# Kernel tuning notes

Hardware: AMD Instinct MI355X
Metric: run time of the kernel (lower is better)

## Reference

```python
import jax, jax.numpy as jnp
import numpy as np
from math import exp

WINDOW_SIZE = 11
SIGMA = 1.5
L_VAL = 1.0


def _make_window(window_size=WINDOW_SIZE, sigma=SIGMA):
    g = np.array([exp(-(x - window_size // 2) ** 2 / float(2 * sigma ** 2))
                  for x in range(window_size)], dtype=np.float32)
    g = g / g.sum()
    w2d = np.outer(g, g).astype(np.float32)  # [K,K]
    return jnp.asarray(w2d)


def _depthwise_gauss(x, w2d):
    # x: [B,C,H,W]; w2d: [K,K]. Depthwise (grouped) conv, SAME padding.
    C = x.shape[1]
    K = w2d.shape[0]
    kern = jnp.broadcast_to(w2d[None, None], (C, 1, K, K))  # OIHW, groups=C
    pad = K // 2
    return jax.lax.conv_general_dilated(
        x, kern,
        window_strides=(1, 1),
        padding=[(pad, pad), (pad, pad)],
        dimension_numbers=('NCHW', 'OIHW', 'NCHW'),
        feature_group_count=C)


def setup_inputs() -> dict:
    key = jax.random.key(0)
    k1, k2 = jax.random.split(key)
    shape = (16, 3, 512, 512)
    img1 = jax.random.uniform(k1, shape, dtype=jnp.float32)
    img2 = jax.random.uniform(k2, shape, dtype=jnp.float32)
    return {"img1": img1, "img2": img2}


def reference(img1, img2):
    w2d = _make_window().astype(img1.dtype)
    mu1 = _depthwise_gauss(img1, w2d)
    mu2 = _depthwise_gauss(img2, w2d)
    mu1_sq = mu1 * mu1
    mu2_sq = mu2 * mu2
    mu1_mu2 = mu1 * mu2
    sigma1_sq = _depthwise_gauss(img1 * img1, w2d) - mu1_sq
    sigma2_sq = _depthwise_gauss(img2 * img2, w2d) - mu2_sq
    sigma12 = _depthwise_gauss(img1 * img2, w2d) - mu1_mu2
    C1 = (0.01 * L_VAL) ** 2
    C2 = (0.03 * L_VAL) ** 2
    ssim_map = ((2 * mu1_mu2 + C1) * (2 * sigma12 + C2)) / \
               ((mu1_sq + mu2_sq + C1) * (sigma1_sq + sigma2_sq + C2))
    return 1.0 - jnp.mean(ssim_map)  # asloss=True, reduction='mean'
```

## Files before the change

### kernel.cpp

```cpp
#include <hip/hip_runtime.h>
#include <math.h>


#define KW 11
#define RAD 5
#define TILE_W 64
#define TILE_H 32
#define IN_W (TILE_W + 2 * RAD)
#define IN_H (TILE_H + 2 * RAD)
#define S_STRIDE 76
#define H_STRIDE 65
#define IMG_H 512
#define IMG_W 512
#define NPLANES 48
#define TILES_X (IMG_W / TILE_W)
#define TILES_Y (IMG_H / TILE_H)
#define NBLOCKS (TILES_X * TILES_Y * NPLANES)
#define NPIX (16.0f * 3.0f * 512.0f * 512.0f)

struct GaussW { float g[KW]; };

__global__ __launch_bounds__(256, 2) void ssim_tile(
    const float* __restrict__ img1, const float* __restrict__ img2,
    float* __restrict__ partial, GaussW W)
{
    __shared__ float s1[IN_H][S_STRIDE];
    __shared__ float s2[IN_H][S_STRIDE];
    __shared__ float h[5][IN_H][H_STRIDE];
    __shared__ float red[4];

    const int tid = threadIdx.x;
    const int plane = blockIdx.y;
    const int tile = blockIdx.x;
    const int tx = tile & (TILES_X - 1);
    const int ty = tile >> 3;
    const int c0 = tx * TILE_W;
    const int r0 = ty * TILE_H;
    const float* __restrict__ p1 = img1 + (size_t)plane * IMG_H * IMG_W;
    const float* __restrict__ p2 = img2 + (size_t)plane * IMG_H * IMG_W;

    for (int idx = tid; idx < IN_H * IN_W; idx += 256) {
        int row = idx / IN_W;
        int col = idx - row * IN_W;
        int gr = r0 - RAD + row;
        int gc = c0 - RAD + col;
        float v1 = 0.f, v2 = 0.f;
        if ((unsigned)gr < (unsigned)IMG_H && (unsigned)gc < (unsigned)IMG_W) {
            v1 = p1[gr * IMG_W + gc];
            v2 = p2[gr * IMG_W + gc];
        }
        s1[row][col] = v1;
        s2[row][col] = v2;
    }
    __syncthreads();

    {
        const int cg = (tid & 7) * 8;
        const int row0 = tid >> 3;
        for (int rr = 0; rr < 2; ++rr) {
            const int row = row0 + rr * 32;
            if (row < IN_H) {
                float ax[8]  = {0,0,0,0,0,0,0,0};
                float ay[8]  = {0,0,0,0,0,0,0,0};
                float axx[8] = {0,0,0,0,0,0,0,0};
                float ayy[8] = {0,0,0,0,0,0,0,0};
                float axy[8] = {0,0,0,0,0,0,0,0};
                #pragma unroll
                for (int j = 0; j < 18; ++j) {
                    float x = s1[row][cg + j];
                    float y = s2[row][cg + j];
                    float xx = x * x, yy = y * y, xy = x * y;
                    #pragma unroll
                    for (int o = 0; o < 8; ++o) {
                        const int t = j - o;
                        if (t >= 0 && t < KW) {
                            const float w = W.g[t];
                            ax[o]  += w * x;
                            ay[o]  += w * y;
                            axx[o] += w * xx;
                            ayy[o] += w * yy;
                            axy[o] += w * xy;
                        }
                    }
                }
                #pragma unroll
                for (int o = 0; o < 8; ++o) {
                    const int col = cg + o;
                    h[0][row][col] = ax[o];
                    h[1][row][col] = ay[o];
                    h[2][row][col] = axx[o];
                    h[3][row][col] = ayy[o];
                    h[4][row][col] = axy[o];
                }
            }
        }
    }
    __syncthreads();

    const int col = tid & 63;
    const int rbase = (tid >> 6) * 8;
    float ox[8]  = {0,0,0,0,0,0,0,0};
    float oy[8]  = {0,0,0,0,0,0,0,0};
    float oxx[8] = {0,0,0,0,0,0,0,0};
    float oyy[8] = {0,0,0,0,0,0,0,0};
    float oxy[8] = {0,0,0,0,0,0,0,0};
    #pragma unroll
    for (int m = 0; m < 18; ++m) {
        const int hr = rbase + m;
        float vx  = h[0][hr][col];
        float vy  = h[1][hr][col];
        float vxx = h[2][hr][col];
        float vyy = h[3][hr][col];
        float vxy = h[4][hr][col];
        #pragma unroll
        for (int o = 0; o < 8; ++o) {
            const int t = m - o;
            if (t >= 0 && t < KW) {
                const float w = W.g[t];
                ox[o]  += w * vx;
                oy[o]  += w * vy;
                oxx[o] += w * vxx;
                oyy[o] += w * vyy;
                oxy[o] += w * vxy;
            }
        }
    }

    const float C1 = 1.0e-4f;
    const float C2 = 9.0e-4f;
    float ssum = 0.f;
    #pragma unroll
    for (int o = 0; o < 8; ++o) {
        float mu1 = ox[o], mu2 = oy[o];
        float mu1sq = mu1 * mu1;
        float mu2sq = mu2 * mu2;
        float mu12  = mu1 * mu2;
        float sg1 = oxx[o] - mu1sq;
        float sg2 = oyy[o] - mu2sq;
        float sg12 = oxy[o] - mu12;
        float num = (2.f * mu12 + C1) * (2.f * sg12 + C2);
        float den = (mu1sq + mu2sq + C1) * (sg1 + sg2 + C2);
        ssum += num / den;
    }

    #pragma unroll
    for (int off = 32; off > 0; off >>= 1)
        ssum += __shfl_down(ssum, off, 64);
    const int lane = tid & 63;
    const int wv = tid >> 6;
    if (lane == 0) red[wv] = ssum;
    __syncthreads();
    if (tid == 0)
        partial[(size_t)blockIdx.y * gridDim.x + blockIdx.x] =
            red[0] + red[1] + red[2] + red[3];
}

__global__ void ssim_finish(const float* __restrict__ partial,
                            float* __restrict__ out)
{
    __shared__ float red[4];
    float s = 0.f;
    for (int i = threadIdx.x; i < NBLOCKS; i += 256) s += partial[i];
    #pragma unroll
    for (int off = 32; off > 0; off >>= 1)
        s += __shfl_down(s, off, 64);
    if ((threadIdx.x & 63) == 0) red[threadIdx.x >> 6] = s;
    __syncthreads();
    if (threadIdx.x == 0) {
        float tot = red[0] + red[1] + red[2] + red[3];
        out[0] = 1.0f - tot / NPIX;
    }
}

extern "C" void kernel_launch(void* const* d_in, const int* in_sizes, int n_in,
                              void* d_out, int out_size, void* d_ws, size_t ws_size,
                              hipStream_t stream) {
    const float* img1 = (const float*)d_in[0];
    const float* img2 = (const float*)d_in[1];
    float* out = (float*)d_out;
    float* partial = (float*)d_ws;

    GaussW W;
    double gd[KW], sum = 0.0;
    for (int i = 0; i < KW; ++i) {
        double d = (double)(i - KW / 2);
        gd[i] = exp(-(d * d) / (2.0 * 1.5 * 1.5));
        sum += gd[i];
    }
    for (int i = 0; i < KW; ++i) W.g[i] = (float)(gd[i] / sum);

    dim3 grid(TILES_X * TILES_Y, NPLANES);
    ssim_tile<<<grid, 256, 0, stream>>>(img1, img2, partial, W);
    ssim_finish<<<1, 256, 0, stream>>>(partial, out);
}
```

Baseline: 233.5 us.

## Read inputs directly from global, store half-precision intermediates, fuse final reduction

Drops the shared-memory staging of the input tiles: each thread reads its 18-element row segment straight from global memory, with a fast path for interior columns. The horizontal-pass intermediates for mu and squared moments are stored as packed half2 in shared memory, with only the cross term kept in float, which cuts LDS footprint and lets launch bounds rise to 4 blocks per CU. The separate finish kernel is replaced by an atomic accumulate with a last-block-done counter, plus a memset of the workspace before launch. Half-precision storage of the second moments risks accuracy loss in the variance subtraction, and the atomic float sum makes the result order-dependent.

```diff
diff --git a/kernel.cpp b/kernel.cpp
--- a/kernel.cpp
+++ b/kernel.cpp
@@ -1,4 +1,5 @@
 #include <hip/hip_runtime.h>
+#include <hip/hip_fp16.h>
 #include <math.h>
 
 
@@ -6,92 +7,90 @@
 #define RAD 5
 #define TILE_W 64
 #define TILE_H 32
-#define IN_W (TILE_W + 2 * RAD)
 #define IN_H (TILE_H + 2 * RAD)
-#define S_STRIDE 76
-#define H_STRIDE 65
+#define HS 65
 #define IMG_H 512
 #define IMG_W 512
 #define NPLANES 48
-#define TILES_X (IMG_W / TILE_W)
-#define TILES_Y (IMG_H / TILE_H)
-#define NBLOCKS (TILES_X * TILES_Y * NPLANES)
-#define NPIX (16.0f * 3.0f * 512.0f * 512.0f)
+#define NBLOCKS (8 * 16 * NPLANES)
+#define NPIXF (16.0f * 3.0f * 512.0f * 512.0f)
 
 struct GaussW { float g[KW]; };
 
-__global__ __launch_bounds__(256, 2) void ssim_tile(
+__global__ __launch_bounds__(256, 4) void ssim_fused(
     const float* __restrict__ img1, const float* __restrict__ img2,
-    float* __restrict__ partial, GaussW W)
+    float* __restrict__ accum, unsigned* __restrict__ count,
+    float* __restrict__ out, GaussW W)
 {
-    __shared__ float s1[IN_H][S_STRIDE];
-    __shared__ float s2[IN_H][S_STRIDE];
-    __shared__ float h[5][IN_H][H_STRIDE];
-    __shared__ float red[4];
+    __shared__ __half2 hxy[IN_H][HS];
+    __shared__ __half2 hxxyy[IN_H][HS];
+    __shared__ float   hxys[IN_H][HS];
+    __shared__ float   red[4];
 
     const int tid = threadIdx.x;
     const int plane = blockIdx.y;
     const int tile = blockIdx.x;
-    const int tx = tile & (TILES_X - 1);
+    const int tx = tile & 7;
     const int ty = tile >> 3;
     const int c0 = tx * TILE_W;
     const int r0 = ty * TILE_H;
-    const float* __restrict__ p1 = img1 + (size_t)plane * IMG_H * IMG_W;
-    const float* __restrict__ p2 = img2 + (size_t)plane * IMG_H * IMG_W;
+    const float* __restrict__ p1 = img1 + (size_t)plane * (IMG_H * IMG_W);
+    const float* __restrict__ p2 = img2 + (size_t)plane * (IMG_H * IMG_W);
 
-    for (int idx = tid; idx < IN_H * IN_W; idx += 256) {
-        int row = idx / IN_W;
-        int col = idx - row * IN_W;
-        int gr = r0 - RAD + row;
-        int gc = c0 - RAD + col;
-        float v1 = 0.f, v2 = 0.f;
-        if ((unsigned)gr < (unsigned)IMG_H && (unsigned)gc < (unsigned)IMG_W) {
-            v1 = p1[gr * IMG_W + gc];
-            v2 = p2[gr * IMG_W + gc];
-        }
-        s1[row][col] = v1;
-        s2[row][col] = v2;
-    }
-    __syncthreads();
+    const bool colsafe = (c0 >= RAD) && (c0 + 68 < IMG_W);
 
-    {
-        const int cg = (tid & 7) * 8;
-        const int row0 = tid >> 3;
-        for (int rr = 0; rr < 2; ++rr) {
-            const int row = row0 + rr * 32;
-            if (row < IN_H) {
-                float ax[8]  = {0,0,0,0,0,0,0,0};
-                float ay[8]  = {0,0,0,0,0,0,0,0};
-                float axx[8] = {0,0,0,0,0,0,0,0};
-                float ayy[8] = {0,0,0,0,0,0,0,0};
-                float axy[8] = {0,0,0,0,0,0,0,0};
+    const int cg = (tid & 7) * 8;
+    const int row0 = tid >> 3;
+    #pragma unroll
+    for (int rr = 0; rr < 2; ++rr) {
+        const int row = row0 + rr * 32;
+        if (row < IN_H) {
+            const int gr = r0 - RAD + row;
+            const bool rowok = (unsigned)gr < (unsigned)IMG_H;
+            const int gc0 = c0 - RAD + cg;
+            const float* a = p1 + (ptrdiff_t)gr * IMG_W + gc0;
+            const float* b = p2 + (ptrdiff_t)gr * IMG_W + gc0;
+
+            float ax[8] = {}, ay[8] = {}, axx[8] = {}, ayy[8] = {}, axy[8] = {};
+
+            auto taps = [&](int j, float xv, float yv) {
+                const float xx = xv * xv, yy = yv * yv, xy = xv * yv;
+                #pragma unroll
+                for (int o = 0; o < 8; ++o) {
+                    const int t = j - o;
+                    if (t >= 0 && t < KW) {
+                        const float w = W.g[t];
+                        ax[o]  += w * xv;
+                        ay[o]  += w * yv;
+                        axx[o] += w * xx;
+                        ayy[o] += w * yy;
+                        axy[o] += w * xy;
+                    }
+                }
+            };
+
+            if (rowok && colsafe) {
+                #pragma unroll
+                for (int j = 0; j < 18; ++j)
+                    taps(j, a[j], b[j]);
+            } else if (rowok) {
                 #pragma unroll
                 for (int j = 0; j < 18; ++j) {
-                    float x = s1[row][cg + j];
-                    float y = s2[row][cg + j];
-                    float xx = x * x, yy = y * y, xy = x * y;
-                    #pragma unroll
-                    for (int o = 0; o < 8; ++o) {
-                        const int t = j - o;
-                        if (t >= 0 && t < KW) {
-                            const float w = W.g[t];
-                            ax[o]  += w * x;
-                            ay[o]  += w * y;
-                            axx[o] += w * xx;
-                            ayy[o] += w * yy;
-                            axy[o] += w * xy;
-                        }
+                    float xv = 0.f, yv = 0.f;
+                    if ((unsigned)(gc0 + j) < (unsigned)IMG_W) {
+                        xv = a[j];
+                        yv = b[j];
                     }
+                    taps(j, xv, yv);
                 }
-                #pragma unroll
-                for (int o = 0; o < 8; ++o) {
-                    const int col = cg + o;
-                    h[0][row][col] = ax[o];
-                    h[1][row][col] = ay[o];
-                    h[2][row][col] = axx[o];
-                    h[3][row][col] = ayy[o];
-                    h[4][row][col] = axy[o];
-                }
+            }
+
+            #pragma unroll
+            for (int o = 0; o < 8; ++o) {
+                const int col = cg + o;
+                hxy[row][col]   = __floats2half2_rn(ax[o], ay[o]);
+                hxxyy[row][col] = __floats2half2_rn(axx[o], ayy[o]);
+                hxys[row][col]  = axy[o];
             }
         }
     }
@@ -99,29 +98,23 @@
 
     const int col = tid & 63;
     const int rbase = (tid >> 6) * 8;
-    float ox[8]  = {0,0,0,0,0,0,0,0};
-    float oy[8]  = {0,0,0,0,0,0,0,0};
-    float oxx[8] = {0,0,0,0,0,0,0,0};
-    float oyy[8] = {0,0,0,0,0,0,0,0};
-    float oxy[8] = {0,0,0,0,0,0,0,0};
+    float ox[8] = {}, oy[8] = {}, oxx[8] = {}, oyy[8] = {}, oxy[8] = {};
     #pragma unroll
     for (int m = 0; m < 18; ++m) {
         const int hr = rbase + m;
-        float vx  = h[0][hr][col];
-        float vy  = h[1][hr][col];
-        float vxx = h[2][hr][col];
-        float vyy = h[3][hr][col];
-        float vxy = h[4][hr][col];
+        const float2 f01 = __half22float2(hxy[hr][col]);
+        const float2 f23 = __half22float2(hxxyy[hr][col]);
+        const float v4 = hxys[hr][col];
         #pragma unroll
         for (int o = 0; o < 8; ++o) {
             const int t = m - o;
             if (t >= 0 && t < KW) {
                 const float w = W.g[t];
-                ox[o]  += w * vx;
-                oy[o]  += w * vy;
-                oxx[o] += w * vxx;
-                oyy[o] += w * vyy;
-                oxy[o] += w * vxy;
+                ox[o]  += w * f01.x;
+                oy[o]  += w * f01.y;
+                oxx[o] += w * f23.x;
+                oyy[o] += w * f23.y;
+                oxy[o] += w * v4;
             }
         }
     }
@@ -131,44 +124,33 @@
     float ssum = 0.f;
     #pragma unroll
     for (int o = 0; o < 8; ++o) {
-        float mu1 = ox[o], mu2 = oy[o];
-        float mu1sq = mu1 * mu1;
-        float mu2sq = mu2 * mu2;
-        float mu12  = mu1 * mu2;
-        float sg1 = oxx[o] - mu1sq;
-        float sg2 = oyy[o] - mu2sq;
-        float sg12 = oxy[o] - mu12;
-        float num = (2.f * mu12 + C1) * (2.f * sg12 + C2);
-        float den = (mu1sq + mu2sq + C1) * (sg1 + sg2 + C2);
+        const float mu1 = ox[o], mu2 = oy[o];
+        const float mu1sq = mu1 * mu1;
+        const float mu2sq = mu2 * mu2;
+        const float mu12  = mu1 * mu2;
+        const float sg1  = oxx[o] - mu1sq;
+        const float sg2  = oyy[o] - mu2sq;
+        const float sg12 = oxy[o] - mu12;
+        const float num = (2.f * mu12 + C1) * (2.f * sg12 + C2);
+        const float den = (mu1sq + mu2sq + C1) * (sg1 + sg2 + C2);
         ssum += num / den;
     }
 
     #pragma unroll
     for (int off = 32; off > 0; off >>= 1)
         ssum += __shfl_down(ssum, off, 64);
-    const int lane = tid & 63;
-    const int wv = tid >> 6;
-    if (lane == 0) red[wv] = ssum;
+    if ((tid & 63) == 0) red[tid >> 6] = ssum;
     __syncthreads();
-    if (tid == 0)
-        partial[(size_t)blockIdx.y * gridDim.x + blockIdx.x] =
-            red[0] + red[1] + red[2] + red[3];
-}
-
-__global__ void ssim_finish(const float* __restrict__ partial,
-                            float* __restrict__ out)
-{
-    __shared__ float red[4];
-    float s = 0.f;
-    for (int i = threadIdx.x; i < NBLOCKS; i += 256) s += partial[i];
-    #pragma unroll
-    for (int off = 32; off > 0; off >>= 1)
-        s += __shfl_down(s, off, 64);
-    if ((threadIdx.x & 63) == 0) red[threadIdx.x >> 6] = s;
-    __syncthreads();
-    if (threadIdx.x == 0) {
-        float tot = red[0] + red[1] + red[2] + red[3];
-        out[0] = 1.0f - tot / NPIX;
+    if (tid == 0) {
+        const float bsum = red[0] + red[1] + red[2] + red[3];
+        atomicAdd(accum, bsum);
+        __threadfence();
+        const unsigned prev = atomicAdd(count, 1u);
+        if (prev == (unsigned)(NBLOCKS - 1)) {
+            __threadfence();
+            const float tot = atomicAdd(accum, 0.0f);
+            out[0] = 1.0f - tot / NPIXF;
+        }
     }
 }
 
@@ -178,18 +160,20 @@
     const float* img1 = (const float*)d_in[0];
     const float* img2 = (const float*)d_in[1];
     float* out = (float*)d_out;
-    float* partial = (float*)d_ws;
+    float* accum = (float*)d_ws;
+    unsigned* count = (unsigned*)d_ws + 2;
+
+    hipMemsetAsync(d_ws, 0, 16, stream);
 
     GaussW W;
     double gd[KW], sum = 0.0;
     for (int i = 0; i < KW; ++i) {
-        double d = (double)(i - KW / 2);
+        const double d = (double)(i - KW / 2);
         gd[i] = exp(-(d * d) / (2.0 * 1.5 * 1.5));
         sum += gd[i];
     }
     for (int i = 0; i < KW; ++i) W.g[i] = (float)(gd[i] / sum);
 
-    dim3 grid(TILES_X * TILES_Y, NPLANES);
-    ssim_tile<<<grid, 256, 0, stream>>>(img1, img2, partial, W);
-    ssim_finish<<<1, 256, 0, stream>>>(partial, out);
+    dim3 grid(8 * 16, NPLANES);
+    ssim_fused<<<grid, 256, 0, stream>>>(img1, img2, accum, count, out, W);
 }
```

After: 412.4 us. +76.6%, slower.
